# Kernel tuning notes

Hardware: AMD Instinct MI355X
Metric: run time of the kernel (lower is better)

## Reference

```python
import jax, jax.numpy as jnp
import numpy as np

E = 1024
H = 16
D = E // H  # head dim 64
B = 2
S = 2048


def setup_inputs() -> dict:
    key = jax.random.key(0)
    k1, k2, k3, k4, k5 = jax.random.split(key, 5)
    scale = 1.0 / np.sqrt(E)
    return {
        "x": jax.random.normal(k1, (B, S, E), dtype=jnp.float32),
        "W_in": jax.random.normal(k2, (E, 3 * E), dtype=jnp.float32) * scale,
        "b_in": jnp.zeros((3 * E,), dtype=jnp.float32),
        "W_out": jax.random.normal(k3, (E, E), dtype=jnp.float32) * scale,
        "b_out": jnp.zeros((E,), dtype=jnp.float32),
        "causal_mask": 1,
    }


def reference(x, W_in, b_in, W_out, b_out, causal_mask):
    b, s, e = x.shape
    qkv = x @ W_in + b_in                      # [B,S,3E]
    q, k, v = jnp.split(qkv, 3, axis=-1)
    # [B,S,E] -> [B,H,S,D]
    q = q.reshape(b, s, H, D).transpose(0, 2, 1, 3)
    k = k.reshape(b, s, H, D).transpose(0, 2, 1, 3)
    v = v.reshape(b, s, H, D).transpose(0, 2, 1, 3)
    scores = jnp.einsum("bhqd,bhkd->bhqk", q, k)
    if causal_mask:
        # mask applied before scaling in the original; -inf is scale-invariant
        mask = jnp.triu(jnp.ones((s, s), dtype=bool), k=1)
        scores = jnp.where(mask, -jnp.inf, scores)
    scores = scores / np.sqrt(D)
    weight = jax.nn.softmax(scores, axis=-1)
    out = jnp.einsum("bhqk,bhkd->bhqd", weight, v)   # [B,H,S,D]
    out = out.transpose(0, 2, 1, 3).reshape(b, s, e)
    return out @ W_out + b_out
```

## Files before the change

kernel.cpp:

```cpp
#include <hip/hip_runtime.h>
#include <hip/hip_bf16.h>
#include <cmath>

typedef __bf16 bf16;
typedef __attribute__((ext_vector_type(8))) __bf16 bf16x8;
typedef __attribute__((ext_vector_type(4))) __bf16 bf16x4;
typedef __attribute__((ext_vector_type(4))) float f32x4;
typedef __attribute__((ext_vector_type(16))) float f32x16;
typedef unsigned int u32;

constexpr int S  = 2048;
constexpr int E  = 1024;
constexpr int H  = 16;
constexpr int D  = 64;
constexpr int B  = 2;
constexpr int M  = B * S;
constexpr int N3 = 3 * E;

static __device__ __forceinline__ void gload16(const void* g, void* l) {
  __builtin_amdgcn_global_load_lds((const __attribute__((address_space(1))) void*)g,
                                   (__attribute__((address_space(3))) void*)l, 16, 0, 0);
}

static __device__ __forceinline__ u32 pack2(float a, float b) {
  union { bf16 h[2]; u32 u; } r;
  r.h[0] = (bf16)a; r.h[1] = (bf16)b;
  return r.u;
}
typedef union { u32 w[4]; bf16x8 v; } FU;

__global__ void k_cvt(const float* __restrict__ in, bf16* __restrict__ out) {
  const int i = (blockIdx.x * blockDim.x + threadIdx.x) * 4;
  const float4 v = *(const float4*)(in + i);
  bf16x4 o = { (bf16)v.x, (bf16)v.y, (bf16)v.z, (bf16)v.w };
  *(bf16x4*)(out + i) = o;
}

__global__ void k_transpose_cvt(const float* __restrict__ in, bf16* __restrict__ out,
                                int R, int C) {
  __shared__ float t[32][33];
  const int c0 = blockIdx.x * 32, r0 = blockIdx.y * 32;
  const int tx = threadIdx.x, ty = threadIdx.y;
  #pragma unroll
  for (int j = 0; j < 32; j += 8)
    t[ty + j][tx] = in[(size_t)(r0 + ty + j) * C + c0 + tx];
  __syncthreads();
  #pragma unroll
  for (int j = 0; j < 32; j += 8)
    out[(size_t)(c0 + ty + j) * R + r0 + tx] = (bf16)t[tx][ty + j];
}

template<int EPI>
__global__ __launch_bounds__(256) void k_gemm(
    const bf16* __restrict__ A, const bf16* __restrict__ Bt,
    const float* __restrict__ bias, float* __restrict__ outF,
    bf16* __restrict__ oQ, bf16* __restrict__ oK, bf16* __restrict__ oV,
    int Kdim, int Nn)
{
  __shared__ __align__(16) char smem[65536];
  const int tid = threadIdx.x;
  const int lane = tid & 63, w = tid >> 6;
  const int lane15 = lane & 15, quad = lane >> 4;
  const int wm = w >> 1, wn = w & 1;

  const int nbx = Nn >> 7;
  const int nwg = gridDim.x;
  const int bid = blockIdx.x;
  const int swz = (bid & 7) * (nwg >> 3) + (bid >> 3);
  const int bn0 = (swz % nbx) * 128;
  const int bm0 = (swz / nbx) * 128;

  const int so0 = w * 1024 + lane * 16;
  int srow[4], slk[4];
  #pragma unroll
  for (int p = 0; p < 4; ++p) {
    const int o = p * 4096 + so0;
    const int row = o >> 7, cbyte = o & 127;
    srow[p] = row;
    slk[p] = (cbyte ^ ((row & 7) << 4)) >> 1;
  }

  f32x4 acc[4][4] = {};
  const int nkt = Kdim >> 6;

  #pragma unroll
  for (int p = 0; p < 4; ++p) {
    gload16(A  + (size_t)(bm0 + srow[p]) * Kdim + slk[p], smem +         p * 4096 + w * 1024);
    gload16(Bt + (size_t)(bn0 + srow[p]) * Kdim + slk[p], smem + 32768 + p * 4096 + w * 1024);
  }

  #pragma unroll 1
  for (int kt = 0; kt < nkt; ++kt) {
    const int cur = kt & 1;
    __builtin_amdgcn_s_barrier();
    if (kt + 1 < nkt) {
      const int k0 = (kt + 1) << 6;
      const int nb = (cur ^ 1) * 16384;
      #pragma unroll
      for (int p = 0; p < 4; ++p) {
        gload16(A  + (size_t)(bm0 + srow[p]) * Kdim + k0 + slk[p],
                smem + nb +         p * 4096 + w * 1024);
        gload16(Bt + (size_t)(bn0 + srow[p]) * Kdim + k0 + slk[p],
                smem + nb + 32768 + p * 4096 + w * 1024);
      }
      asm volatile("s_waitcnt vmcnt(8)" ::: "memory");
    } else {
      asm volatile("s_waitcnt vmcnt(0)" ::: "memory");
    }
    __builtin_amdgcn_s_barrier();

    const char* cA = smem + cur * 16384;
    const char* cB = smem + 32768 + cur * 16384;
    #pragma unroll
    for (int kk = 0; kk < 2; ++kk) {
      bf16x8 af[4], bfr[4];
      #pragma unroll
      for (int f = 0; f < 4; ++f) {
        const int ra = wm * 64 + f * 16 + lane15;
        af[f] = *(const bf16x8*)(cA + ra * 128 +
                 ((kk * 64 + (quad << 4)) ^ ((ra & 7) << 4)));
        const int rb = wn * 64 + f * 16 + lane15;
        bfr[f] = *(const bf16x8*)(cB + rb * 128 +
                 ((kk * 64 + (quad << 4)) ^ ((rb & 7) << 4)));
      }
      #pragma unroll
      for (int i = 0; i < 4; ++i)
        #pragma unroll
        for (int j = 0; j < 4; ++j)
          acc[i][j] = __builtin_amdgcn_mfma_f32_16x16x32_bf16(af[i], bfr[j], acc[i][j], 0, 0, 0);
    }
  }

  if constexpr (EPI == 1) {
    #pragma unroll
    for (int i = 0; i < 4; ++i)
      #pragma unroll
      for (int j = 0; j < 4; ++j) {
        const int n = bn0 + wn * 64 + j * 16 + lane15;
        const float bv = bias[n];
        #pragma unroll
        for (int r = 0; r < 4; ++r) {
          const int m = bm0 + wm * 64 + i * 16 + quad * 4 + r;
          outF[(size_t)m * E + n] = acc[i][j][r] + bv;
        }
      }
  } else {
    const int which = bn0 >> 10;
    const int b  = bm0 >> 11;
    const int s0 = bm0 & (S - 1);
    const int cn0 = bn0 & (E - 1);
    if (which < 2) {
      bf16* dst = (which == 0) ? oQ : oK;
      __builtin_amdgcn_s_barrier();
      char* lC = smem;
      #pragma unroll
      for (int j = 0; j < 4; ++j) {
        const int n_loc = wn * 64 + j * 16 + lane15;
        const float bv = bias[bn0 + n_loc];
        #pragma unroll
        for (int i = 0; i < 4; ++i)
          #pragma unroll
          for (int r = 0; r < 4; ++r) {
            const int m_loc = wm * 64 + i * 16 + quad * 4 + r;
            *(bf16*)(lC + m_loc * 256 + ((n_loc * 2) ^ ((m_loc & 7) << 4))) =
                (bf16)(acc[i][j][r] + bv);
          }
      }
      __builtin_amdgcn_s_barrier();
      const int h0 = cn0 >> 6;
      #pragma unroll
      for (int it = 0; it < 8; ++it) {
        const int cch = w * 64 + it * 8 + (lane >> 3);
        const int m_loc = cch >> 1, hh = cch & 1, piece = lane & 7;
        const bf16x8 vv = *(const bf16x8*)(lC + m_loc * 256 +
                          ((hh * 128 + piece * 16) ^ ((m_loc & 7) << 4)));
        *(bf16x8*)(dst + ((size_t)(b * H + h0 + hh) * S + s0 + m_loc) * D + piece * 8) = vv;
      }
    } else {
      #pragma unroll
      for (int j = 0; j < 4; ++j) {
        const int n_loc = wn * 64 + j * 16 + lane15;
        const int cn = cn0 + n_loc;
        const int h = cn >> 6, d = cn & 63;
        const float bv = bias[bn0 + n_loc];
        bf16* base = oV + ((size_t)(b * H + h) * D + d) * S + s0 + wm * 64;
        #pragma unroll
        for (int i = 0; i < 4; ++i) {
          bf16x4 pk = { (bf16)(acc[i][j][0] + bv), (bf16)(acc[i][j][1] + bv),
                        (bf16)(acc[i][j][2] + bv), (bf16)(acc[i][j][3] + bv) };
          *(bf16x4*)(base + i * 16 + quad * 4) = pk;
        }
      }
    }
  }
}

__global__ __launch_bounds__(256, 2) void k_attn(
    const bf16* __restrict__ Qb, const bf16* __restrict__ Kb, const bf16* __restrict__ Vt,
    bf16* __restrict__ AO, const int* __restrict__ cmask)
{
  __shared__ __align__(16) char lK[2][64 * 128];
  __shared__ __align__(16) char lV[2][64 * 128];
  __shared__ __align__(16) float corr_lds[4][32];
  __shared__ __align__(16) float lrow_lds[4][32];

  const int tid = threadIdx.x, lane = tid & 63, w = tid >> 6;
  const int h = lane >> 5, q31 = lane & 31;
  const int bh = blockIdx.x;
  const int c  = 15 - (int)blockIdx.y;
  const int causal = cmask[0];
  const int q0w = c * 128 + 32 * w;
  const int qg  = q0w + q31;
  const int nkt   = causal ? (2 * c + 2) : (S / 64);
  const int nkt_w = causal ? (2 * c + 1 + (w >> 1)) : (S / 64);
  const float S2 = 0.18033688011112042f;

  const bf16* Qh = Qb + (size_t)bh * S * D;
  const bf16* Kh = Kb + (size_t)bh * S * D;
  const bf16* Vh = Vt + (size_t)bh * D * S;

  const int so0 = w * 1024 + lane * 16;
  int srow[2], slk[2];
  #pragma unroll
  for (int p = 0; p < 2; ++p) {
    const int o = p * 4096 + so0;
    const int row = o >> 7, cb = o & 127;
    srow[p] = row;
    slk[p] = (cb ^ ((row & 7) << 4)) >> 1;
  }

  bf16x8 qf[4];
  #pragma unroll
  for (int ds = 0; ds < 4; ++ds)
    qf[ds] = *(const bf16x8*)(Qh + (size_t)qg * D + 16 * ds + 8 * h);

  #pragma unroll
  for (int p = 0; p < 2; ++p) {
    gload16(Kh + (size_t)srow[p] * D + slk[p], lK[0] + p * 4096 + so0);
    gload16(Vh + (size_t)srow[p] * S + slk[p], lV[0] + p * 4096 + so0);
  }

  f32x16 o0 = {}, o1 = {};
  float mrun = -INFINITY, lr = 0.f;
  const int swz = (q31 & 7) << 4;

  #pragma unroll 1
  for (int t = 0; t < nkt; ++t) {
    const int cb = t & 1;
    __builtin_amdgcn_s_barrier();
    if (t + 1 < nkt) {
      const int kb = (t + 1) * 64;
      #pragma unroll
      for (int p = 0; p < 2; ++p) {
        gload16(Kh + (size_t)(kb + srow[p]) * D + slk[p], lK[cb ^ 1] + p * 4096 + so0);
        gload16(Vh + (size_t)srow[p] * S + kb + slk[p],   lV[cb ^ 1] + p * 4096 + so0);
      }
      asm volatile("s_waitcnt vmcnt(4)" ::: "memory");
    } else {
      asm volatile("s_waitcnt vmcnt(0)" ::: "memory");
    }
    __builtin_amdgcn_s_barrier();

    if (t < nkt_w) {
      f32x16 s0v = {}, s1v = {};
      #pragma unroll
      for (int ds = 0; ds < 4; ++ds) {
        const int col = (32 * ds + 16 * h) ^ swz;
        const bf16x8 kf0 = *(const bf16x8*)(lK[cb] + q31 * 128 + col);
        const bf16x8 kf1 = *(const bf16x8*)(lK[cb] + (32 + q31) * 128 + col);
        s0v = __builtin_amdgcn_mfma_f32_32x32x16_bf16(kf0, qf[ds], s0v, 0, 0, 0);
        s1v = __builtin_amdgcn_mfma_f32_32x32x16_bf16(kf1, qf[ds], s1v, 0, 0, 0);
      }

      if (causal && t == nkt_w - 1) {
        #pragma unroll
        for (int r = 0; r < 16; ++r) {
          const int kg = 64 * t + (r & 3) + 8 * (r >> 2) + 4 * h;
          if (kg > qg)      s0v[r] = -INFINITY;
          if (kg + 32 > qg) s1v[r] = -INFINITY;
        }
      }

      float a8[8];
      #pragma unroll
      for (int i = 0; i < 8; ++i)
        a8[i] = fmaxf(fmaxf(s0v[i], s0v[i + 8]), fmaxf(s1v[i], s1v[i + 8]));
      float tmax = fmaxf(fmaxf(fmaxf(a8[0], a8[1]), fmaxf(a8[2], a8[3])),
                         fmaxf(fmaxf(a8[4], a8[5]), fmaxf(a8[6], a8[7])));
      tmax = fmaxf(tmax, __shfl_xor(tmax, 32, 64));

      const bool nogrow = __all(tmax <= mrun);
      const float mnew = nogrow ? mrun : fmaxf(mrun, tmax);
      float corrf = 1.f;
      if (!nogrow) {
        corrf = __builtin_amdgcn_exp2f((mrun - mnew) * S2);
        corr_lds[w][q31] = corrf;
      }
      const float msc = mnew * S2;

      #pragma unroll
      for (int r = 0; r < 16; ++r) {
        s0v[r] = __builtin_amdgcn_exp2f(__builtin_fmaf(s0v[r], S2, -msc));
        s1v[r] = __builtin_amdgcn_exp2f(__builtin_fmaf(s1v[r], S2, -msc));
      }

      float b8[8];
      #pragma unroll
      for (int i = 0; i < 8; ++i)
        b8[i] = (s0v[i] + s0v[i + 8]) + (s1v[i] + s1v[i + 8]);
      float psum = ((b8[0] + b8[1]) + (b8[2] + b8[3])) + ((b8[4] + b8[5]) + (b8[6] + b8[7]));
      psum += __shfl_xor(psum, 32, 64);
      lr = lr * corrf + psum;
      mrun = mnew;

      u32 pk[8][2];
      #pragma unroll
      for (int jj = 0; jj < 4; ++jj) {
        pk[jj][0]     = pack2(s0v[4 * jj],     s0v[4 * jj + 1]);
        pk[jj][1]     = pack2(s0v[4 * jj + 2], s0v[4 * jj + 3]);
        pk[jj + 4][0] = pack2(s1v[4 * jj],     s1v[4 * jj + 1]);
        pk[jj + 4][1] = pack2(s1v[4 * jj + 2], s1v[4 * jj + 3]);
      }

      if (!nogrow) {
        #pragma unroll
        for (int j = 0; j < 4; ++j) {
          const f32x4 cv = *(const f32x4*)&corr_lds[w][8 * j + 4 * h];
          #pragma unroll
          for (int sr = 0; sr < 4; ++sr) {
            o0[4 * j + sr] *= cv[sr];
            o1[4 * j + sr] *= cv[sr];
          }
        }
      }

      #pragma unroll
      for (int ks = 0; ks < 4; ++ks) {
        u32 a0 = pk[2 * ks][0], b0 = pk[2 * ks + 1][0];
        u32 a1 = pk[2 * ks][1], b1 = pk[2 * ks + 1][1];
        asm volatile("v_permlane32_swap_b32 %0, %1" : "+v"(a0), "+v"(b0));
        asm volatile("v_permlane32_swap_b32 %0, %1" : "+v"(a1), "+v"(b1));
        FU f; f.w[0] = a0; f.w[1] = a1; f.w[2] = b0; f.w[3] = b1;
        const int col = (32 * ks + 16 * h) ^ swz;
        const bf16x8 vf0 = *(const bf16x8*)(lV[cb] + q31 * 128 + col);
        const bf16x8 vf1 = *(const bf16x8*)(lV[cb] + (32 + q31) * 128 + col);
        o0 = __builtin_amdgcn_mfma_f32_32x32x16_bf16(f.v, vf0, o0, 0, 0, 0);
        o1 = __builtin_amdgcn_mfma_f32_32x32x16_bf16(f.v, vf1, o1, 0, 0, 0);
      }
    }
  }

  lrow_lds[w][q31] = lr;
  const int b = bh >> 4, h16 = bh & 15;
  #pragma unroll
  for (int j = 0; j < 4; ++j) {
    const f32x4 lv = *(const f32x4*)&lrow_lds[w][8 * j + 4 * h];
    #pragma unroll
    for (int sr = 0; sr < 4; ++sr) {
      const int r = 4 * j + sr;
      const float inv = 1.0f / lv[sr];
      const int qrow = q0w + (r & 3) + 8 * (r >> 2) + 4 * h;
      bf16* dst = AO + ((size_t)(b * S + qrow)) * E + h16 * D;
      dst[q31]      = (bf16)(o0[r] * inv);
      dst[32 + q31] = (bf16)(o1[r] * inv);
    }
  }
}

extern "C" void kernel_launch(void* const* d_in, const int* in_sizes, int n_in,
                              void* d_out, int out_size, void* d_ws, size_t ws_size,
                              hipStream_t stream) {
  (void)in_sizes; (void)n_in; (void)out_size; (void)ws_size;
  const float* x     = (const float*)d_in[0];
  const float* W_in  = (const float*)d_in[1];
  const float* b_in  = (const float*)d_in[2];
  const float* W_out = (const float*)d_in[3];
  const float* b_out = (const float*)d_in[4];
  const int*   cmask = (const int*)d_in[5];

  char* ws = (char*)d_ws;
  bf16* xb    = (bf16*)ws; ws += (size_t)M * E * 2;
  bf16* wtin  = (bf16*)ws; ws += (size_t)N3 * E * 2;
  bf16* wtout = (bf16*)ws; ws += (size_t)E * E * 2;
  bf16* qB    = (bf16*)ws; ws += (size_t)B * H * S * D * 2;
  bf16* kB    = (bf16*)ws; ws += (size_t)B * H * S * D * 2;
  bf16* vT    = (bf16*)ws; ws += (size_t)B * H * S * D * 2;
  bf16* ao    = (bf16*)ws; ws += (size_t)M * E * 2;

  k_cvt<<<M * E / 1024, 256, 0, stream>>>(x, xb);
  k_transpose_cvt<<<dim3(N3 / 32, E / 32), dim3(32, 8), 0, stream>>>(W_in, wtin, E, N3);
  k_transpose_cvt<<<dim3(E / 32, E / 32), dim3(32, 8), 0, stream>>>(W_out, wtout, E, E);
  k_gemm<0><<<dim3((M / 128) * (N3 / 128)), 256, 0, stream>>>(
      xb, wtin, b_in, nullptr, qB, kB, vT, E, N3);
  k_attn<<<dim3(32, 16), 256, 0, stream>>>(qB, kB, vT, ao, cmask);
  k_gemm<1><<<dim3((M / 128) * (E / 128)), 256, 0, stream>>>(
      ao, wtout, b_out, (float*)d_out, nullptr, nullptr, nullptr, E, E);
}
```

Before: 120.9 us.

## Split causal attention into two balanced KV partial passes and merge with combine kernel

Each attention block now handles two work items: query chunk jb over key tiles [0,jb] and query chunk 15-jb over the remaining key tiles. This evens out causal work across blocks, which previously ranged from 2 to 32 KV tiles. Partial outputs plus running max and sum are written to workspace, and a new k_combine kernel merges them into the attention output. It also adds s_setprio around the MFMA sections. The cost is an extra kernel launch and extra partial-output traffic, with xb reused as scratch.

```diff
diff --git a/kernel.cpp b/kernel.cpp
--- a/kernel.cpp
+++ b/kernel.cpp
@@ -16,6 +16,7 @@
 constexpr int B  = 2;
 constexpr int M  = B * S;
 constexpr int N3 = 3 * E;
+constexpr int NROWS = B * H * S;
 
 static __device__ __forceinline__ void gload16(const void* g, void* l) {
   __builtin_amdgcn_global_load_lds((const __attribute__((address_space(1))) void*)g,
@@ -197,7 +198,8 @@
 
 __global__ __launch_bounds__(256, 2) void k_attn(
     const bf16* __restrict__ Qb, const bf16* __restrict__ Kb, const bf16* __restrict__ Vt,
-    bf16* __restrict__ AO, const int* __restrict__ cmask)
+    bf16* __restrict__ pO0, bf16* __restrict__ pO1,
+    float* __restrict__ pM, float* __restrict__ pL, const int* __restrict__ cmask)
 {
   __shared__ __align__(16) char lK[2][64 * 128];
   __shared__ __align__(16) char lV[2][64 * 128];
@@ -207,12 +209,8 @@
   const int tid = threadIdx.x, lane = tid & 63, w = tid >> 6;
   const int h = lane >> 5, q31 = lane & 31;
   const int bh = blockIdx.x;
-  const int c  = 15 - (int)blockIdx.y;
+  const int jb = blockIdx.y;
   const int causal = cmask[0];
-  const int q0w = c * 128 + 32 * w;
-  const int qg  = q0w + q31;
-  const int nkt   = causal ? (2 * c + 2) : (S / 64);
-  const int nkt_w = causal ? (2 * c + 1 + (w >> 1)) : (S / 64);
   const float S2 = 0.18033688011112042f;
 
   const bf16* Qh = Qb + (size_t)bh * S * D;
@@ -224,147 +222,191 @@
   #pragma unroll
   for (int p = 0; p < 2; ++p) {
     const int o = p * 4096 + so0;
-    const int row = o >> 7, cb = o & 127;
+    const int row = o >> 7, cbv = o & 127;
     srow[p] = row;
-    slk[p] = (cb ^ ((row & 7) << 4)) >> 1;
-  }
-
-  bf16x8 qf[4];
-  #pragma unroll
-  for (int ds = 0; ds < 4; ++ds)
-    qf[ds] = *(const bf16x8*)(Qh + (size_t)qg * D + 16 * ds + 8 * h);
-
-  #pragma unroll
-  for (int p = 0; p < 2; ++p) {
-    gload16(Kh + (size_t)srow[p] * D + slk[p], lK[0] + p * 4096 + so0);
-    gload16(Vh + (size_t)srow[p] * S + slk[p], lV[0] + p * 4096 + so0);
-  }
-
-  f32x16 o0 = {}, o1 = {};
-  float mrun = -INFINITY, lr = 0.f;
+    slk[p] = (cbv ^ ((row & 7) << 4)) >> 1;
+  }
   const int swz = (q31 & 7) << 4;
 
   #pragma unroll 1
-  for (int t = 0; t < nkt; ++t) {
-    const int cb = t & 1;
+  for (int pidx = 0; pidx < 2; ++pidx) {
+    const int c  = pidx ? (15 - jb) : jb;
+    const int t0 = causal ? (pidx ? (c + 1) : 0) : (pidx ? 16 : 0);
+    const int t1 = causal ? (pidx ? (2 * c + 2) : (c + 1)) : (pidx ? 32 : 16);
+    const int q0w = c * 128 + 32 * w;
+    const int qg  = q0w + q31;
+
     __builtin_amdgcn_s_barrier();
-    if (t + 1 < nkt) {
-      const int kb = (t + 1) * 64;
-      #pragma unroll
-      for (int p = 0; p < 2; ++p) {
-        gload16(Kh + (size_t)(kb + srow[p]) * D + slk[p], lK[cb ^ 1] + p * 4096 + so0);
-        gload16(Vh + (size_t)srow[p] * S + kb + slk[p],   lV[cb ^ 1] + p * 4096 + so0);
-      }
-      asm volatile("s_waitcnt vmcnt(4)" ::: "memory");
-    } else {
-      asm volatile("s_waitcnt vmcnt(0)" ::: "memory");
-    }
-    __builtin_amdgcn_s_barrier();
-
-    if (t < nkt_w) {
-      f32x16 s0v = {}, s1v = {};
-      #pragma unroll
-      for (int ds = 0; ds < 4; ++ds) {
-        const int col = (32 * ds + 16 * h) ^ swz;
-        const bf16x8 kf0 = *(const bf16x8*)(lK[cb] + q31 * 128 + col);
-        const bf16x8 kf1 = *(const bf16x8*)(lK[cb] + (32 + q31) * 128 + col);
-        s0v = __builtin_amdgcn_mfma_f32_32x32x16_bf16(kf0, qf[ds], s0v, 0, 0, 0);
-        s1v = __builtin_amdgcn_mfma_f32_32x32x16_bf16(kf1, qf[ds], s1v, 0, 0, 0);
-      }
-
-      if (causal && t == nkt_w - 1) {
+
+    bf16x8 qf[4];
+    #pragma unroll
+    for (int ds = 0; ds < 4; ++ds)
+      qf[ds] = *(const bf16x8*)(Qh + (size_t)qg * D + 16 * ds + 8 * h);
+
+    #pragma unroll
+    for (int p = 0; p < 2; ++p) {
+      gload16(Kh + (size_t)(t0 * 64 + srow[p]) * D + slk[p], lK[0] + p * 4096 + so0);
+      gload16(Vh + (size_t)srow[p] * S + t0 * 64 + slk[p],   lV[0] + p * 4096 + so0);
+    }
+
+    f32x16 o0 = {}, o1 = {};
+    float mrun = -INFINITY, lr = 0.f;
+
+    #pragma unroll 1
+    for (int t = t0; t < t1; ++t) {
+      const int cb = (t - t0) & 1;
+      __builtin_amdgcn_s_barrier();
+      if (t + 1 < t1) {
+        const int kb = (t + 1) * 64;
+        #pragma unroll
+        for (int p = 0; p < 2; ++p) {
+          gload16(Kh + (size_t)(kb + srow[p]) * D + slk[p], lK[cb ^ 1] + p * 4096 + so0);
+          gload16(Vh + (size_t)srow[p] * S + kb + slk[p],   lV[cb ^ 1] + p * 4096 + so0);
+        }
+        asm volatile("s_waitcnt vmcnt(4)" ::: "memory");
+      } else {
+        asm volatile("s_waitcnt vmcnt(0)" ::: "memory");
+      }
+      __builtin_amdgcn_s_barrier();
+
+      const bool active = !causal || (64 * t <= q0w + 31);
+      if (active) {
+        f32x16 s0v = {}, s1v = {};
+        __builtin_amdgcn_s_setprio(1);
+        #pragma unroll
+        for (int ds = 0; ds < 4; ++ds) {
+          const int col = (32 * ds + 16 * h) ^ swz;
+          const bf16x8 kf0 = *(const bf16x8*)(lK[cb] + q31 * 128 + col);
+          const bf16x8 kf1 = *(const bf16x8*)(lK[cb] + (32 + q31) * 128 + col);
+          s0v = __builtin_amdgcn_mfma_f32_32x32x16_bf16(kf0, qf[ds], s0v, 0, 0, 0);
+          s1v = __builtin_amdgcn_mfma_f32_32x32x16_bf16(kf1, qf[ds], s1v, 0, 0, 0);
+        }
+        __builtin_amdgcn_s_setprio(0);
+
+        if (causal && (64 * t + 63 > q0w)) {
+          #pragma unroll
+          for (int r = 0; r < 16; ++r) {
+            const int kg = 64 * t + (r & 3) + 8 * (r >> 2) + 4 * h;
+            if (kg > qg)      s0v[r] = -INFINITY;
+            if (kg + 32 > qg) s1v[r] = -INFINITY;
+          }
+        }
+
+        float a8[8];
+        #pragma unroll
+        for (int i = 0; i < 8; ++i)
+          a8[i] = fmaxf(fmaxf(s0v[i], s0v[i + 8]), fmaxf(s1v[i], s1v[i + 8]));
+        float tmax = fmaxf(fmaxf(fmaxf(a8[0], a8[1]), fmaxf(a8[2], a8[3])),
+                           fmaxf(fmaxf(a8[4], a8[5]), fmaxf(a8[6], a8[7])));
+        tmax = fmaxf(tmax, __shfl_xor(tmax, 32, 64));
+
+        const bool nogrow = __all(tmax <= mrun);
+        const float mnew = nogrow ? mrun : fmaxf(mrun, tmax);
+        float corrf = 1.f;
+        if (!nogrow) {
+          corrf = __builtin_amdgcn_exp2f((mrun - mnew) * S2);
+          corr_lds[w][q31] = corrf;
+        }
+        const float msc = mnew * S2;
+
         #pragma unroll
         for (int r = 0; r < 16; ++r) {
-          const int kg = 64 * t + (r & 3) + 8 * (r >> 2) + 4 * h;
-          if (kg > qg)      s0v[r] = -INFINITY;
-          if (kg + 32 > qg) s1v[r] = -INFINITY;
-        }
-      }
-
-      float a8[8];
-      #pragma unroll
-      for (int i = 0; i < 8; ++i)
-        a8[i] = fmaxf(fmaxf(s0v[i], s0v[i + 8]), fmaxf(s1v[i], s1v[i + 8]));
-      float tmax = fmaxf(fmaxf(fmaxf(a8[0], a8[1]), fmaxf(a8[2], a8[3])),
-                         fmaxf(fmaxf(a8[4], a8[5]), fmaxf(a8[6], a8[7])));
-      tmax = fmaxf(tmax, __shfl_xor(tmax, 32, 64));
-
-      const bool nogrow = __all(tmax <= mrun);
-      const float mnew = nogrow ? mrun : fmaxf(mrun, tmax);
-      float corrf = 1.f;
-      if (!nogrow) {
-        corrf = __builtin_amdgcn_exp2f((mrun - mnew) * S2);
-        corr_lds[w][q31] = corrf;
-      }
-      const float msc = mnew * S2;
-
-      #pragma unroll
-      for (int r = 0; r < 16; ++r) {
-        s0v[r] = __builtin_amdgcn_exp2f(__builtin_fmaf(s0v[r], S2, -msc));
-        s1v[r] = __builtin_amdgcn_exp2f(__builtin_fmaf(s1v[r], S2, -msc));
-      }
-
-      float b8[8];
-      #pragma unroll
-      for (int i = 0; i < 8; ++i)
-        b8[i] = (s0v[i] + s0v[i + 8]) + (s1v[i] + s1v[i + 8]);
-      float psum = ((b8[0] + b8[1]) + (b8[2] + b8[3])) + ((b8[4] + b8[5]) + (b8[6] + b8[7]));
-      psum += __shfl_xor(psum, 32, 64);
-      lr = lr * corrf + psum;
-      mrun = mnew;
-
-      u32 pk[8][2];
-      #pragma unroll
-      for (int jj = 0; jj < 4; ++jj) {
-        pk[jj][0]     = pack2(s0v[4 * jj],     s0v[4 * jj + 1]);
-        pk[jj][1]     = pack2(s0v[4 * jj + 2], s0v[4 * jj + 3]);
-        pk[jj + 4][0] = pack2(s1v[4 * jj],     s1v[4 * jj + 1]);
-        pk[jj + 4][1] = pack2(s1v[4 * jj + 2], s1v[4 * jj + 3]);
-      }
-
-      if (!nogrow) {
-        #pragma unroll
-        for (int j = 0; j < 4; ++j) {
-          const f32x4 cv = *(const f32x4*)&corr_lds[w][8 * j + 4 * h];
+          s0v[r] = __builtin_amdgcn_exp2f(__builtin_fmaf(s0v[r], S2, -msc));
+          s1v[r] = __builtin_amdgcn_exp2f(__builtin_fmaf(s1v[r], S2, -msc));
+        }
+
+        float b8[8];
+        #pragma unroll
+        for (int i = 0; i < 8; ++i)
+          b8[i] = (s0v[i] + s0v[i + 8]) + (s1v[i] + s1v[i + 8]);
+        float psum = ((b8[0] + b8[1]) + (b8[2] + b8[3])) + ((b8[4] + b8[5]) + (b8[6] + b8[7]));
+        psum += __shfl_xor(psum, 32, 64);
+        lr = lr * corrf + psum;
+        mrun = mnew;
+
+        u32 pk[8][2];
+        #pragma unroll
+        for (int jj = 0; jj < 4; ++jj) {
+          pk[jj][0]     = pack2(s0v[4 * jj],     s0v[4 * jj + 1]);
+          pk[jj][1]     = pack2(s0v[4 * jj + 2], s0v[4 * jj + 3]);
+          pk[jj + 4][0] = pack2(s1v[4 * jj],     s1v[4 * jj + 1]);
+          pk[jj + 4][1] = pack2(s1v[4 * jj + 2], s1v[4 * jj + 3]);
+        }
+
+        if (!nogrow) {
           #pragma unroll
-          for (int sr = 0; sr < 4; ++sr) {
-            o0[4 * j + sr] *= cv[sr];
-            o1[4 * j + sr] *= cv[sr];
+          for (int j = 0; j < 4; ++j) {
+            const f32x4 cv = *(const f32x4*)&corr_lds[w][8 * j + 4 * h];
+            #pragma unroll
+            for (int sr = 0; sr < 4; ++sr) {
+              o0[4 * j + sr] *= cv[sr];
+              o1[4 * j + sr] *= cv[sr];
+            }
           }
         }
-      }
-
-      #pragma unroll
-      for (int ks = 0; ks < 4; ++ks) {
-        u32 a0 = pk[2 * ks][0], b0 = pk[2 * ks + 1][0];
-        u32 a1 = pk[2 * ks][1], b1 = pk[2 * ks + 1][1];
-        asm volatile("v_permlane32_swap_b32 %0, %1" : "+v"(a0), "+v"(b0));
-        asm volatile("v_permlane32_swap_b32 %0, %1" : "+v"(a1), "+v"(b1));
-        FU f; f.w[0] = a0; f.w[1] = a1; f.w[2] = b0; f.w[3] = b1;
-        const int col = (32 * ks + 16 * h) ^ swz;
-        const bf16x8 vf0 = *(const bf16x8*)(lV[cb] + q31 * 128 + col);
-        const bf16x8 vf1 = *(const bf16x8*)(lV[cb] + (32 + q31) * 128 + col);
-        o0 = __builtin_amdgcn_mfma_f32_32x32x16_bf16(f.v, vf0, o0, 0, 0, 0);
-        o1 = __builtin_amdgcn_mfma_f32_32x32x16_bf16(f.v, vf1, o1, 0, 0, 0);
-      }
-    }
-  }
-
-  lrow_lds[w][q31] = lr;
-  const int b = bh >> 4, h16 = bh & 15;
-  #pragma unroll
-  for (int j = 0; j < 4; ++j) {
-    const f32x4 lv = *(const f32x4*)&lrow_lds[w][8 * j + 4 * h];
+
+        __builtin_amdgcn_s_setprio(1);
+        #pragma unroll
+        for (int ks = 0; ks < 4; ++ks) {
+          u32 a0 = pk[2 * ks][0], b0 = pk[2 * ks + 1][0];
+          u32 a1 = pk[2 * ks][1], b1 = pk[2 * ks + 1][1];
+          asm volatile("v_permlane32_swap_b32 %0, %1" : "+v"(a0), "+v"(b0));
+          asm volatile("v_permlane32_swap_b32 %0, %1" : "+v"(a1), "+v"(b1));
+          FU f; f.w[0] = a0; f.w[1] = a1; f.w[2] = b0; f.w[3] = b1;
+          const int col = (32 * ks + 16 * h) ^ swz;
+          const bf16x8 vf0 = *(const bf16x8*)(lV[cb] + q31 * 128 + col);
+          const bf16x8 vf1 = *(const bf16x8*)(lV[cb] + (32 + q31) * 128 + col);
+          o0 = __builtin_amdgcn_mfma_f32_32x32x16_bf16(f.v, vf0, o0, 0, 0, 0);
+          o1 = __builtin_amdgcn_mfma_f32_32x32x16_bf16(f.v, vf1, o1, 0, 0, 0);
+        }
+        __builtin_amdgcn_s_setprio(0);
+      }
+    }
+
+    if (h == 0) {
+      pM[(size_t)pidx * NROWS + bh * S + qg] = mrun;
+      pL[(size_t)pidx * NROWS + bh * S + qg] = lr;
+    }
+    lrow_lds[w][q31] = lr;
+    bf16* po = pidx ? pO1 : pO0;
     #pragma unroll
-    for (int sr = 0; sr < 4; ++sr) {
-      const int r = 4 * j + sr;
-      const float inv = 1.0f / lv[sr];
-      const int qrow = q0w + (r & 3) + 8 * (r >> 2) + 4 * h;
-      bf16* dst = AO + ((size_t)(b * S + qrow)) * E + h16 * D;
-      dst[q31]      = (bf16)(o0[r] * inv);
-      dst[32 + q31] = (bf16)(o1[r] * inv);
-    }
-  }
+    for (int j = 0; j < 4; ++j) {
+      const f32x4 lv = *(const f32x4*)&lrow_lds[w][8 * j + 4 * h];
+      #pragma unroll
+      for (int sr = 0; sr < 4; ++sr) {
+        const int r = 4 * j + sr;
+        const float inv = lv[sr] > 0.f ? 1.0f / lv[sr] : 0.f;
+        const int qrow = q0w + (r & 3) + 8 * (r >> 2) + 4 * h;
+        bf16* dst = po + ((size_t)(bh * S + qrow)) * D;
+        dst[q31]      = (bf16)(o0[r] * inv);
+        dst[32 + q31] = (bf16)(o1[r] * inv);
+      }
+    }
+  }
+}
+
+__global__ __launch_bounds__(256) void k_combine(
+    const bf16* __restrict__ pO0, const bf16* __restrict__ pO1,
+    const float* __restrict__ pM, const float* __restrict__ pL,
+    bf16* __restrict__ AO)
+{
+  const float S2 = 0.18033688011112042f;
+  const int idx = blockIdx.x * 256 + threadIdx.x;
+  const int row = idx >> 3, d0 = (idx & 7) * 8;
+  const float mA = pM[row], mB = pM[NROWS + row];
+  const float lA = pL[row], lB = pL[NROWS + row];
+  const float m = fmaxf(mA, mB);
+  const float wA = lA > 0.f ? lA * __builtin_amdgcn_exp2f((mA - m) * S2) : 0.f;
+  const float wB = lB > 0.f ? lB * __builtin_amdgcn_exp2f((mB - m) * S2) : 0.f;
+  const float inv = 1.0f / (wA + wB);
+  const bf16x8 a = *(const bf16x8*)(pO0 + (size_t)row * D + d0);
+  const bf16x8 b = *(const bf16x8*)(pO1 + (size_t)row * D + d0);
+  bf16x8 o;
+  #pragma unroll
+  for (int i = 0; i < 8; ++i)
+    o[i] = (bf16)((wA * (float)a[i] + wB * (float)b[i]) * inv);
+  const int bb = row >> 15, hh = (row >> 11) & 15, s = row & 2047;
+  *(bf16x8*)(AO + ((size_t)(bb * S + s)) * E + hh * D + d0) = o;
 }
 
 extern "C" void kernel_launch(void* const* d_in, const int* in_sizes, int n_in,
@@ -386,13 +428,18 @@
   bf16* kB    = (bf16*)ws; ws += (size_t)B * H * S * D * 2;
   bf16* vT    = (bf16*)ws; ws += (size_t)B * H * S * D * 2;
   bf16* ao    = (bf16*)ws; ws += (size_t)M * E * 2;
+  bf16* pO1   = (bf16*)ws; ws += (size_t)NROWS * D * 2;
+  float* pMb  = (float*)ws; ws += (size_t)2 * NROWS * 4;
+  float* pLb  = (float*)ws; ws += (size_t)2 * NROWS * 4;
+  bf16* pO0   = xb;
 
   k_cvt<<<M * E / 1024, 256, 0, stream>>>(x, xb);
   k_transpose_cvt<<<dim3(N3 / 32, E / 32), dim3(32, 8), 0, stream>>>(W_in, wtin, E, N3);
   k_transpose_cvt<<<dim3(E / 32, E / 32), dim3(32, 8), 0, stream>>>(W_out, wtout, E, E);
   k_gemm<0><<<dim3((M / 128) * (N3 / 128)), 256, 0, stream>>>(
       xb, wtin, b_in, nullptr, qB, kB, vT, E, N3);
-  k_attn<<<dim3(32, 16), 256, 0, stream>>>(qB, kB, vT, ao, cmask);
+  k_attn<<<dim3(32, 16), 256, 0, stream>>>(qB, kB, vT, pO0, pO1, pMb, pLb, cmask);
+  k_combine<<<NROWS * 8 / 256, 256, 0, stream>>>(pO0, pO1, pMb, pLb, ao);
   k_gemm<1><<<dim3((M / 128) * (E / 128)), 256, 0, stream>>>(
       ao, wtout, b_out, (float*)d_out, nullptr, nullptr, nullptr, E, E);
 }
```

New measurement: 115.0 us. -4.9%, faster.
